# Kernel optimization log

Measured on AMD Instinct MI355X. Metric: run time of the kernel, lower is better.

Reference implementation:

```python
import jax, jax.numpy as jnp
import numpy as np

K_NN = 8        # neighbors
RADIUS = 0.1    # neighbor distance cutoff


def setup_inputs() -> dict:
    key = jax.random.key(0)
    k1, k2 = jax.random.split(key)
    B, N, KS = 2, 8192, 16  # batch, points, mask slots
    pc = jax.random.uniform(k1, (B, N, 3), dtype=jnp.float32)
    mask = jax.random.uniform(k2, (B, N, KS), dtype=jnp.float32)
    return {"pc": pc, "mask": mask}


def _knn(k, pc):
    # squared pairwise distances via gemm: (B,N,N)
    sq = jnp.sum(pc * pc, axis=-1)
    d2 = sq[:, :, None] + sq[:, None, :] - 2.0 * jnp.einsum("bnd,bmd->bnm", pc, pc)
    d2 = jnp.maximum(d2, 0.0)
    neg_d2, idx = jax.lax.top_k(-d2, k)          # k smallest distances
    dist = jnp.sqrt(jnp.maximum(-neg_d2, 0.0))   # (B,N,k) euclidean
    return dist, idx


def reference(pc, mask):
    # mask: (B,N,KS) -> (B,KS,N)
    mask_t = jnp.transpose(mask, (0, 2, 1))
    dist, idx = _knn(K_NN, pc)                   # (B,N,k) each
    # replace out-of-radius neighbors with the self index (nearest = self)
    self_idx = idx[:, :, :1]                     # (B,N,1)
    idx = jnp.where(dist > RADIUS, self_idx, idx)
    idx = jax.lax.stop_gradient(idx)
    # grouping_operation: (B,KS,N) gathered at (B,N,k) -> (B,KS,N,k)
    nn_mask = jax.vmap(lambda f, i: f[:, i])(mask_t, idx)
    # loss_norm=1: L1 norm over mask-slot dim (dim=1), mean over k, mean overall
    diff = mask_t[:, :, :, None] - nn_mask       # (B,KS,N,k)
    loss = jnp.sum(jnp.abs(diff), axis=1).mean(axis=-1)  # (B,N)
    return loss.mean()
```

## Files before the change

### kernel.cpp

```cpp
#include <hip/hip_runtime.h>

#define BATCH 2
#define NPTS  8192
#define KS    16
#define KNN   8
#define R2LOOSE 0.0101f
#define KEYMASK 0xFFFFE000u
#define NCELL   1000
#define CSTRIDE 1024

#define QB       64
#define NWAVE    8
#define NTHREADS 512
#define CAP      32
#define NBLK     (BATCH * NPTS / QB)

__device__ __forceinline__ int cell_of(float x, float y, float z) {
    int cx = (int)(x * 10.0f); cx = cx > 9 ? 9 : cx;
    int cy = (int)(y * 10.0f); cy = cy > 9 ? 9 : cy;
    int cz = (int)(z * 10.0f); cz = cz > 9 ? 9 : cz;
    return (cx * 10 + cy) * 10 + cz;
}

__global__ void count_kernel(const float* __restrict__ pc, int* cfill) {
    const int i = blockIdx.x * 1024 + threadIdx.x;
    const float x = pc[3 * i], y = pc[3 * i + 1], z = pc[3 * i + 2];
    const int b = i >> 13;
    atomicAdd(&cfill[b * CSTRIDE + cell_of(x, y, z)], 1);
}

__global__ __launch_bounds__(1024) void scan_kernel(int* cfill, int* cstart,
                                                    float* out) {
    __shared__ int arr[1024];
    const int b = blockIdx.x, t = threadIdx.x;
    if (b == 0 && t == 0) out[0] = 0.0f;
    const int cnt = cfill[b * CSTRIDE + t];
    arr[t] = cnt;
    __syncthreads();
    for (int off = 1; off < 1024; off <<= 1) {
        const int v = (t >= off) ? arr[t - off] : 0;
        __syncthreads();
        arr[t] += v;
        __syncthreads();
    }
    const int excl = arr[t] - cnt;
    cstart[b * CSTRIDE + t] = excl;
    cfill[b * CSTRIDE + t]  = excl;
}

__global__ void scatter_kernel(const float* __restrict__ pc,
                               float4* __restrict__ cs,
                               int* __restrict__ sidx, int* cfill) {
    const int i = blockIdx.x * 1024 + threadIdx.x;
    const float x = pc[3 * i], y = pc[3 * i + 1], z = pc[3 * i + 2];
    const int b = i >> 13;
    const float sq = fmaf(z, z, fmaf(y, y, x * x));
    const int pos = atomicAdd(&cfill[b * CSTRIDE + cell_of(x, y, z)], 1);
    cs[b * NPTS + pos]   = make_float4(x, y, z, -0.5f * sq);
    sidx[b * NPTS + pos] = i & (NPTS - 1);
}

__global__ __launch_bounds__(512) void knn_loss_kernel(
    const float4* __restrict__ cs,
    const int*    __restrict__ sidx,
    const int*    __restrict__ cstart,
    const float*  __restrict__ mask,
    float* __restrict__ out)
{
    __shared__ unsigned sbuf[CAP * NTHREADS];
    __shared__ int      fidx[QB * KNN];
    __shared__ int      qid[QB];
    __shared__ float    red[NWAVE];

    const int t = threadIdx.x;
    const int q = t & (QB - 1);
    const int s = t >> 6;
    const int su = __builtin_amdgcn_readfirstlane(s);
    const int blk = blockIdx.x;
    const int b  = blk >> 7;
    const int q0 = (blk & 127) * QB;
    const int qpos = q0 + q;

    const float4* csb = cs + b * NPTS;
    const float4 qc = csb[qpos];
    const int    qi = sidx[b * NPTS + qpos];
    if (s == 0) qid[q] = qi;

    const float qx = qc.x, qy = qc.y, qz = qc.z;
    const float qs = -2.0f * qc.w;
    const float negthr = (qs - R2LOOSE) * 0.5f;
    const unsigned SENT = (__float_as_uint(R2LOOSE) & KEYMASK) | 0x1FFFu;

    int lex = cell_of(qx, qy, qz);
    int cmn = lex, cmx = lex;
#pragma unroll
    for (int off = 32; off; off >>= 1) {
        cmn = min(cmn, __shfl_xor(cmn, off));
        cmx = max(cmx, __shfl_xor(cmx, off));
    }
    const int cfirst = __builtin_amdgcn_readfirstlane(cmn);
    const int clast  = __builtin_amdgcn_readfirstlane(cmx);

    int lo0 = cfirst - 111, h0 = clast - 89;
    int lo1 = cfirst - 11,  h1 = clast + 11;
    int lo2 = cfirst + 89,  h2 = clast + 111;
    lo0 = min(max(lo0, 0), 1000);
    lo1 = min(max(lo1, 0), 1000);
    lo2 = min(max(lo2, 0), 1000);
    int hp0 = min(max(h0 + 1, 0), 1000);
    int hp1 = min(max(h1 + 1, 0), 1000);
    int hp2 = min(max(h2 + 1, 0), 1000);
    lo1 = max(lo1, hp0);
    lo2 = max(lo2, hp1);

    const int* csp = cstart + b * CSTRIDE;
    const int P0 = csp[lo0], E0 = csp[hp0];
    const int P1 = csp[lo1], E1 = csp[hp1];
    const int P2 = csp[lo2], E2 = csp[hp2];
    const int L0 = max(0, E0 - P0);
    const int L1 = max(0, E1 - P1);
    const int L2 = max(0, E2 - P2);

    int cnt = 0;
    auto EVAL = [&](const float4& c, int spos) {
        const float tt = fmaf(c.x, qx, fmaf(c.y, qy, fmaf(c.z, qz, c.w)));
        const float d2 = fmaxf(fmaf(-2.0f, tt, qs), 0.0f);
        const unsigned key =
            (__float_as_uint(d2) & KEYMASK) | (unsigned)spos;
        const int slot = cnt < (CAP - 1) ? cnt : (CAP - 1);
        sbuf[slot * NTHREADS + t] = key;
        cnt += (tt >= negthr) ? 1 : 0;
    };
    auto SCAN = [&](int P, int L) {
        int j = (su * L) >> 3;
        const int e = ((su + 1) * L) >> 3;
        for (; j + 4 <= e; j += 4) {
            const float4 c0 = csb[P + j];
            const float4 c1 = csb[P + j + 1];
            const float4 c2 = csb[P + j + 2];
            const float4 c3 = csb[P + j + 3];
            EVAL(c0, P + j);     EVAL(c1, P + j + 1);
            EVAL(c2, P + j + 2); EVAL(c3, P + j + 3);
        }
        for (; j < e; ++j) { const float4 c0 = csb[P + j]; EVAL(c0, P + j); }
    };
    SCAN(P0, L0);
    SCAN(P1, L1);
    SCAN(P2, L2);

    unsigned md[KNN];
#pragma unroll
    for (int k = 0; k < KNN; ++k) md[k] = SENT;
    const int m = cnt < CAP ? cnt : CAP;
    for (int k = 0; k < m; ++k) {
        unsigned ky = sbuf[k * NTHREADS + t];
#pragma unroll
        for (int i = 0; i < KNN; ++i) {
            const unsigned mn = min(ky, md[i]);
            const unsigned mx = max(ky, md[i]);
            md[i] = mn; ky = mx;
        }
    }
    __syncthreads();

    {
        uint4* bp = (uint4*)&sbuf[t * KNN];
        bp[0] = make_uint4(md[0], md[1], md[2], md[3]);
        bp[1] = make_uint4(md[4], md[5], md[6], md[7]);
    }
    __syncthreads();

    if (s == 0) {
        for (int l = 1; l < NWAVE; ++l) {
            const uint4* lp = (const uint4*)&sbuf[(l * QB + q) * KNN];
            const uint4 r0 = lp[0], r1 = lp[1];
            const unsigned tk[8] = {r0.x, r0.y, r0.z, r0.w,
                                    r1.x, r1.y, r1.z, r1.w};
#pragma unroll
            for (int k = 0; k < 8; ++k) {
                unsigned ky = tk[k];
                if (ky < md[KNN - 1]) {
#pragma unroll
                    for (int i = 0; i < KNN; ++i) {
                        const unsigned mn = min(ky, md[i]);
                        const unsigned mx = max(ky, md[i]);
                        md[i] = mn; ky = mx;
                    }
                }
            }
        }
#pragma unroll
        for (int k = 0; k < KNN; ++k) {
            const unsigned ky = md[k];
            int nb;
            if (ky >= SENT) {
                nb = qi;
            } else {
                const int sp = (int)(ky & 0x1FFFu);
                const float4 cc = csb[sp];
                const float dx = cc.x - qx;
                const float dy = cc.y - qy;
                const float dz = cc.z - qz;
                const float d2 = fmaf(dx, dx, fmaf(dy, dy, dz * dz));
                nb = (sqrtf(d2) > 0.1f) ? qi : sidx[b * NPTS + sp];
            }
            fidx[q * KNN + k] = nb;
        }
    }
    __syncthreads();

    const int q2 = t >> 3;
    const int j2 = t & 7;
    const int qg = qid[q2];
    const int nb = fidx[q2 * KNN + j2];
    const float* mrow = mask + ((size_t)b * NPTS + qg) * KS;
    const float* nrow = mask + ((size_t)b * NPTS + nb) * KS;
    float acc = 0.0f;
#pragma unroll
    for (int c = 0; c < KS; c += 4) {
        const float4 a = *(const float4*)(mrow + c);
        const float4 v = *(const float4*)(nrow + c);
        acc += fabsf(a.x - v.x) + fabsf(a.y - v.y) +
               fabsf(a.z - v.z) + fabsf(a.w - v.w);
    }

#pragma unroll
    for (int off = 32; off > 0; off >>= 1) acc += __shfl_down(acc, off);
    if ((t & 63) == 0) red[s] = acc;
    __syncthreads();
    if (t == 0) {
        float sum = 0.0f;
#pragma unroll
        for (int i = 0; i < NWAVE; ++i) sum += red[i];
        atomicAdd(out, sum * (1.0f / (BATCH * NPTS * KNN)));
    }
}

extern "C" void kernel_launch(void* const* d_in, const int* in_sizes, int n_in,
                              void* d_out, int out_size, void* d_ws, size_t ws_size,
                              hipStream_t stream) {
    const float* pc   = (const float*)d_in[0];
    const float* mask = (const float*)d_in[1];
    float* out = (float*)d_out;

    float4* cs     = (float4*)d_ws;
    int*    sidx   = (int*)((char*)d_ws + 262144);
    int*    cstart = (int*)((char*)d_ws + 327680);
    int*    cfill  = (int*)((char*)d_ws + 335872);

    hipMemsetAsync(cfill, 0, 2 * CSTRIDE * sizeof(int), stream);
    hipLaunchKernelGGL(count_kernel,   dim3(16), dim3(1024), 0, stream, pc, cfill);
    hipLaunchKernelGGL(scan_kernel,    dim3(2),  dim3(1024), 0, stream,
                       cfill, cstart, out);
    hipLaunchKernelGGL(scatter_kernel, dim3(16), dim3(1024), 0, stream,
                       pc, cs, sidx, cfill);
    hipLaunchKernelGGL(knn_loss_kernel, dim3(NBLK), dim3(512), 0, stream,
                       cs, sidx, cstart, mask, out);
}
```

Baseline: 87.58 us.

## Stage candidate cell points through shared-memory tiles in kNN scan

Instead of each wave reading candidate float4 points directly from global memory per cell range, the block cooperatively loads the concatenated three cell ranges into a shared tile of 1024 points, with their sorted indices, and waves scan their slice from LDS. This aims to replace redundant uniform global loads with a single coalesced load per tile. It adds 20KB of LDS on top of the existing 64KB sort buffer, which may reduce occupancy, plus two barriers per tile and index-selection arithmetic.

```diff
diff --git a/kernel.cpp b/kernel.cpp
--- a/kernel.cpp
+++ b/kernel.cpp
@@ -13,6 +13,7 @@
 #define NWAVE    8
 #define NTHREADS 512
 #define CAP      32
+#define TILEC    1024
 #define NBLK     (BATCH * NPTS / QB)
 
 __device__ __forceinline__ int cell_of(float x, float y, float z) {
@@ -67,6 +68,8 @@
     const float*  __restrict__ mask,
     float* __restrict__ out)
 {
+    __shared__ float4   tile[TILEC];
+    __shared__ int      tsp[TILEC];
     __shared__ unsigned sbuf[CAP * NTHREADS];
     __shared__ int      fidx[QB * KNN];
     __shared__ int      qid[QB];
@@ -120,6 +123,7 @@
     const int L0 = max(0, E0 - P0);
     const int L1 = max(0, E1 - P1);
     const int L2 = max(0, E2 - P2);
+    const int C  = L0 + L1 + L2;
 
     int cnt = 0;
     auto EVAL = [&](const float4& c, int spos) {
@@ -131,22 +135,31 @@
         sbuf[slot * NTHREADS + t] = key;
         cnt += (tt >= negthr) ? 1 : 0;
     };
-    auto SCAN = [&](int P, int L) {
-        int j = (su * L) >> 3;
-        const int e = ((su + 1) * L) >> 3;
+
+    for (int tb = 0; tb < C; tb += TILEC) {
+        const int nt = min(TILEC, C - tb);
+        for (int p = t; p < nt; p += NTHREADS) {
+            const int g = tb + p;
+            int sp = P0 + g;
+            sp = (g >= L0)      ? (P1 + (g - L0))      : sp;
+            sp = (g >= L0 + L1) ? (P2 + (g - L0 - L1)) : sp;
+            tile[p] = csb[sp];
+            tsp[p]  = sp;
+        }
+        __syncthreads();
+
+        int j = (su * nt) >> 3;
+        const int e = ((su + 1) * nt) >> 3;
         for (; j + 4 <= e; j += 4) {
-            const float4 c0 = csb[P + j];
-            const float4 c1 = csb[P + j + 1];
-            const float4 c2 = csb[P + j + 2];
-            const float4 c3 = csb[P + j + 3];
-            EVAL(c0, P + j);     EVAL(c1, P + j + 1);
-            EVAL(c2, P + j + 2); EVAL(c3, P + j + 3);
-        }
-        for (; j < e; ++j) { const float4 c0 = csb[P + j]; EVAL(c0, P + j); }
-    };
-    SCAN(P0, L0);
-    SCAN(P1, L1);
-    SCAN(P2, L2);
+            const float4 c0 = tile[j],     c1 = tile[j + 1];
+            const float4 c2 = tile[j + 2], c3 = tile[j + 3];
+            const int s0 = tsp[j],     s1 = tsp[j + 1];
+            const int s2 = tsp[j + 2], s3 = tsp[j + 3];
+            EVAL(c0, s0); EVAL(c1, s1); EVAL(c2, s2); EVAL(c3, s3);
+        }
+        for (; j < e; ++j) { const float4 c0 = tile[j]; EVAL(c0, tsp[j]); }
+        __syncthreads();
+    }
 
     unsigned md[KNN];
 #pragma unroll
```

Result: faster. 84.03 us (-4.0%).
